# Kernel tuning notes

Hardware: AMD Instinct MI355X
Metric: run time of the kernel (lower is better)

## Reference

```python
import jax, jax.numpy as jnp
import numpy as np

D_IN = 3072      # == d_out (code reshapes x directly into heads)
D_OUT = 3072
N_HEADS = 16
HEAD_DIM = D_OUT // N_HEADS          # 192
D_C = D_OUT // 3                     # 1024, compressed latent dim
LN_EPS = 1e-5


def setup_inputs() -> dict:
    key = jax.random.key(0)
    ks = jax.random.split(key, 8)
    s = 0.02
    return {
        "x": jax.random.normal(ks[0], (2, 2048, D_IN), dtype=jnp.float32),
        "W_query": jax.random.normal(ks[1], (D_OUT, D_IN), dtype=jnp.float32) * s,
        "W_kv": jax.random.normal(ks[2], (D_C, D_IN), dtype=jnp.float32) * s,
        "W_uk": jax.random.normal(ks[3], (D_OUT, D_C), dtype=jnp.float32) * s,
        "W_uv": jax.random.normal(ks[4], (D_OUT, D_C), dtype=jnp.float32) * s,
        "W_out": jax.random.normal(ks[5], (D_OUT, D_OUT), dtype=jnp.float32) * s,
        "b_out": jnp.zeros((D_OUT,), dtype=jnp.float32),
        "ln_g": jnp.ones((D_C,), dtype=jnp.float32),
        "ln_b": jnp.zeros((D_C,), dtype=jnp.float32),
    }


def reference(x, W_query, W_kv, W_uk, W_uv, W_out, b_out, ln_g, ln_b):
    B, T, D = x.shape
    past_length = 0  # prefill, kv_cache=None

    # absorbed K projection: (d_out, d_in) @ (d_out, d_c) -> (H, head_dim, d_c)
    absorbed_k = (W_query @ W_uk).reshape(N_HEADS, HEAD_DIM, D_C)

    # compressed latent c_kv = LayerNorm(x @ W_kv^T), shape (B, S, d_c)
    c = x @ W_kv.T
    mu = jnp.mean(c, axis=-1, keepdims=True)
    var = jnp.mean(jnp.square(c - mu), axis=-1, keepdims=True)
    c_kv = (c - mu) * jax.lax.rsqrt(var + LN_EPS) * ln_g + ln_b
    S = c_kv.shape[1]

    # values decompressed: (B, S, H, head_dim)
    v = (c_kv @ W_uv.T).reshape(B, S, N_HEADS, HEAD_DIM)

    # queries: raw x reshaped into heads (as in the original code)
    q = x.reshape(B, T, N_HEADS, HEAD_DIM)

    # scores in compressed space: q @ absorbed_k @ c_kv^T
    tmp = jnp.einsum("bthd,hdc->bhtc", q, absorbed_k)           # (B,H,T,d_c)
    scores = jnp.einsum("bhtc,bsc->bhts", tmp, c_kv)
    scores = scores / np.float32(np.sqrt(HEAD_DIM))

    # causal mask with past_length offset (tril diagonal=past_length)
    row = jnp.arange(T)[:, None]
    col = jnp.arange(S)[None, :]
    mask = col <= (row + past_length)                            # (T,S) bool
    scores = jnp.where(mask[None, None], scores, -jnp.inf)

    weights = jax.nn.softmax(scores, axis=-1)                    # (B,H,T,S)

    ctx = jnp.einsum("bhts,bshd->bthd", weights, v).reshape(B, T, D_OUT)
    out = ctx @ W_out.T + b_out
    return out, c_kv
```

## Files before the change

kernel.cpp:

```cpp
#include <hip/hip_runtime.h>
#include <hip/hip_bf16.h>
#include <math.h>

#define BB 2
#define TT 2048
#define DD 3072
#define NH 16
#define HD 192
#define DC 1024

typedef __attribute__((ext_vector_type(8))) short bh8;
typedef __attribute__((ext_vector_type(4))) float f32x4;
typedef unsigned int u32;

__device__ __forceinline__ short f2b(float f) {
  __hip_bfloat16 h = __float2bfloat16(f);
  return *reinterpret_cast<short*>(&h);
}

__device__ __forceinline__ void gload16(const void* g, void* lds) {
  __builtin_amdgcn_global_load_lds(
      (const __attribute__((address_space(1))) u32*)g,
      (__attribute__((address_space(3))) u32*)lds, 16, 0, 0);
}

__global__ __launch_bounds__(256) void cast_f2b_k(const float* __restrict__ in,
                                                  short* __restrict__ out) {
  size_t i = ((size_t)blockIdx.x * 256 + threadIdx.x) * 8;
  float4 v0 = *(const float4*)&in[i];
  float4 v1 = *(const float4*)&in[i + 4];
  bh8 o;
  o[0] = f2b(v0.x); o[1] = f2b(v0.y); o[2] = f2b(v0.z); o[3] = f2b(v0.w);
  o[4] = f2b(v1.x); o[5] = f2b(v1.y); o[6] = f2b(v1.z); o[7] = f2b(v1.w);
  *(bh8*)&out[i] = o;
}

__global__ __launch_bounds__(256) void sum_cast_k(const float* __restrict__ p0,
                                                  const float* __restrict__ p1,
                                                  short* __restrict__ out) {
  size_t i = ((size_t)blockIdx.x * 256 + threadIdx.x) * 8;
  float4 a0 = *(const float4*)&p0[i];
  float4 a1 = *(const float4*)&p0[i + 4];
  float4 b0 = *(const float4*)&p1[i];
  float4 b1 = *(const float4*)&p1[i + 4];
  bh8 o;
  o[0] = f2b(a0.x + b0.x); o[1] = f2b(a0.y + b0.y);
  o[2] = f2b(a0.z + b0.z); o[3] = f2b(a0.w + b0.w);
  o[4] = f2b(a1.x + b1.x); o[5] = f2b(a1.y + b1.y);
  o[6] = f2b(a1.z + b1.z); o[7] = f2b(a1.w + b1.w);
  *(bh8*)&out[i] = o;
}

__global__ __launch_bounds__(256) void castT_f2b_k(const float* __restrict__ in,
                                                   short* __restrict__ out,
                                                   int R, int C) {
  __shared__ float t[64][65];
  const int cx = blockIdx.x * 64, ry = blockIdx.y * 64;
  const int tid = threadIdx.x, lx = tid & 15, ly = tid >> 4;
#pragma unroll
  for (int i = 0; i < 4; ++i) {
    int r = ly + i * 16;
    float4 v = *(const float4*)&in[(size_t)(ry + r) * C + cx + lx * 4];
    t[r][lx * 4 + 0] = v.x; t[r][lx * 4 + 1] = v.y;
    t[r][lx * 4 + 2] = v.z; t[r][lx * 4 + 3] = v.w;
  }
  __syncthreads();
#pragma unroll
  for (int i = 0; i < 4; ++i) {
    int c = ly + i * 16;
    ushort4 v;
    v.x = (unsigned short)f2b(t[lx * 4 + 0][c]);
    v.y = (unsigned short)f2b(t[lx * 4 + 1][c]);
    v.z = (unsigned short)f2b(t[lx * 4 + 2][c]);
    v.w = (unsigned short)f2b(t[lx * 4 + 3][c]);
    *(ushort4*)&out[(size_t)(cx + c) * R + ry + lx * 4] = v;
  }
}

template <int OUTMODE, bool BIAS>
__global__ __launch_bounds__(256) void gemm_bf16(
    const short* __restrict__ A, const short* __restrict__ Bt,
    const float* __restrict__ bias, void* __restrict__ Cout,
    void* __restrict__ Cout2,
    int M, int N, int Klen, int lda, int ldb, size_t zoff_bytes) {
  __shared__ short As[8192];
  __shared__ short Bs[8192];
  const int tid = threadIdx.x;
  const int w = tid >> 6, l = tid & 63, lm = l & 15, lg = l >> 4;
  const int wr = w >> 1, wc = w & 1;

  const int bz = blockIdx.z;
  A += (size_t)bz * Klen;
  Bt += (size_t)bz * Klen;
  Cout = (void*)((char*)Cout + (size_t)bz * zoff_bytes);

  const int nwg = gridDim.x * gridDim.y;
  const int flat = blockIdx.y * gridDim.x + blockIdx.x;
  const int wgid = (flat & 7) * (nwg >> 3) + (flat >> 3);
  const int m0 = (wgid / gridDim.x) * 128, n0 = (wgid % gridDim.x) * 128;

  f32x4 acc[4][4] = {};

  for (int k0 = 0; k0 < Klen; k0 += 64) {
    __syncthreads();
#pragma unroll
    for (int c = 0; c < 4; ++c) {
      int p = c * 256 + w * 64 + l;
      int row = p >> 3, kc = p & 7;
      int g = kc ^ (row & 7);
      gload16(&A[(size_t)(m0 + row) * lda + k0 + g * 8],
              &As[(c * 256 + w * 64) * 8]);
      gload16(&Bt[(size_t)(n0 + row) * ldb + k0 + g * 8],
              &Bs[(c * 256 + w * 64) * 8]);
    }
    __syncthreads();

#pragma unroll
    for (int kh = 0; kh < 2; ++kh) {
      bh8 a[4], b[4];
#pragma unroll
      for (int mi = 0; mi < 4; ++mi) {
        int r = wr * 64 + mi * 16 + lm;
        a[mi] = *(const bh8*)&As[r * 64 + (((kh * 4 + lg) ^ (r & 7)) << 3)];
      }
#pragma unroll
      for (int ni = 0; ni < 4; ++ni) {
        int r = wc * 64 + ni * 16 + lm;
        b[ni] = *(const bh8*)&Bs[r * 64 + (((kh * 4 + lg) ^ (r & 7)) << 3)];
      }
#pragma unroll
      for (int mi = 0; mi < 4; ++mi)
#pragma unroll
        for (int ni = 0; ni < 4; ++ni)
          acc[mi][ni] = __builtin_amdgcn_mfma_f32_16x16x32_bf16(
              a[mi], b[ni], acc[mi][ni], 0, 0, 0);
    }
  }

#pragma unroll
  for (int mi = 0; mi < 4; ++mi) {
#pragma unroll
    for (int ni = 0; ni < 4; ++ni) {
      int row = m0 + wr * 64 + mi * 16 + lg * 4;
      int col = n0 + wc * 64 + ni * 16 + lm;
      float bi = 0.f;
      if (BIAS) bi = bias[col];
      if (OUTMODE == 3) {
        if (n0 < 3072) {
          int b = row >> 11, t = row & 2047;
          ushort4 o4;
          o4.x = (unsigned short)f2b(acc[mi][ni][0]);
          o4.y = (unsigned short)f2b(acc[mi][ni][1]);
          o4.z = (unsigned short)f2b(acc[mi][ni][2]);
          o4.w = (unsigned short)f2b(acc[mi][ni][3]);
          *(ushort4*)&((short*)Cout2)[((size_t)(b * DD + col)) * TT + t] = o4;
        } else {
#pragma unroll
          for (int r = 0; r < 4; ++r)
            ((short*)Cout)[(size_t)(row + r) * DD + (col - 3072)] =
                f2b(acc[mi][ni][r]);
        }
      } else {
#pragma unroll
        for (int r = 0; r < 4; ++r) {
          float v = acc[mi][ni][r] + bi;
          if (OUTMODE == 1)
            ((short*)Cout)[(size_t)(row + r) * N + col] = f2b(v);
          else
            ((float*)Cout)[(size_t)(row + r) * N + col] = v;
        }
      }
    }
  }
}

__global__ __launch_bounds__(256) void ln_k(const float* __restrict__ cp0,
                                            const float* __restrict__ cp1,
                                            const float* __restrict__ g,
                                            const float* __restrict__ bta,
                                            float* __restrict__ o32,
                                            short* __restrict__ o16) {
  const int row = blockIdx.x;
  const int tid = threadIdx.x;
  __shared__ float red1[4];
  __shared__ float red2[4];

  float4 va = *(const float4*)&cp0[(size_t)row * DC + tid * 4];
  float4 vb = *(const float4*)&cp1[(size_t)row * DC + tid * 4];
  float4 v;
  v.x = va.x + vb.x; v.y = va.y + vb.y; v.z = va.z + vb.z; v.w = va.w + vb.w;
  float s = v.x + v.y + v.z + v.w;
#pragma unroll
  for (int mk = 32; mk; mk >>= 1) s += __shfl_xor(s, mk, 64);
  if ((tid & 63) == 0) red1[tid >> 6] = s;
  __syncthreads();
  float mu = (red1[0] + red1[1] + red1[2] + red1[3]) * (1.f / DC);

  float dx = v.x - mu, dy = v.y - mu, dz = v.z - mu, dw = v.w - mu;
  float s2 = dx * dx + dy * dy + dz * dz + dw * dw;
#pragma unroll
  for (int mk = 32; mk; mk >>= 1) s2 += __shfl_xor(s2, mk, 64);
  if ((tid & 63) == 0) red2[tid >> 6] = s2;
  __syncthreads();
  float var = (red2[0] + red2[1] + red2[2] + red2[3]) * (1.f / DC);
  float rs = rsqrtf(var + 1e-5f);

  float4 gg = *(const float4*)&g[tid * 4];
  float4 bb = *(const float4*)&bta[tid * 4];
  float4 o;
  o.x = dx * rs * gg.x + bb.x;
  o.y = dy * rs * gg.y + bb.y;
  o.z = dz * rs * gg.z + bb.z;
  o.w = dw * rs * gg.w + bb.w;
  *(float4*)&o32[(size_t)row * DC + tid * 4] = o;
  ushort4 ob;
  ob.x = (unsigned short)f2b(o.x); ob.y = (unsigned short)f2b(o.y);
  ob.z = (unsigned short)f2b(o.z); ob.w = (unsigned short)f2b(o.w);
  *(ushort4*)&o16[(size_t)row * DC + tid * 4] = ob;
}

__global__ __launch_bounds__(256, 4) void attn_mfma(
    const short* __restrict__ xb, const short* __restrict__ kf,
    const short* __restrict__ vT, short* __restrict__ ctx) {
  __shared__ short Ks[64 * 192];
  __shared__ short Vs[192 * 64];
  __shared__ short Ps[4][16 * 64];

  const int idx = blockIdx.x;
  const int qt = 31 - (idx >> 5);
  const int bh = idx & 31;
  const int h = bh & 15, b = bh >> 4;
  const int tid = threadIdx.x, w = tid >> 6, l = tid & 63;
  const int lm = l & 15, lg = l >> 4;
  const int qw0 = qt * 64 + w * 16;
  const float QS = 0.07216878364870323f;

  bh8 qf[6];
  {
    const short* qrow = &xb[(size_t)(b * TT + qw0 + lm) * DD + h * HD];
#pragma unroll
    for (int kq = 0; kq < 6; ++kq)
      qf[kq] = *(const bh8*)&qrow[kq * 32 + lg * 8];
  }

  f32x4 o[12] = {};
  float mrun[4], lrun[4];
#pragma unroll
  for (int r = 0; r < 4; ++r) { mrun[r] = -INFINITY; lrun[r] = 0.f; }

  for (int st = 0; st <= qt; ++st) {
    const int s0 = st * 64;
    __syncthreads();
#pragma unroll
    for (int c = 0; c < 6; ++c) {
      int p = c * 256 + w * 64 + l;
      {
        int krow = p / 24, kc = p - krow * 24;
        int g = kc ^ (krow & 7);
        gload16(&kf[(size_t)(b * TT + s0 + krow) * DD + h * HD + g * 8],
                &Ks[(c * 256 + w * 64) * 8]);
      }
      {
        int vrow = p >> 3, vc = p & 7;
        int gv = vc ^ (vrow & 7);
        gload16(&vT[(size_t)((b * NH + h) * HD + vrow) * TT + s0 + gv * 8],
                &Vs[(c * 256 + w * 64) * 8]);
      }
    }
    __syncthreads();

    f32x4 s[4] = {};
    __builtin_amdgcn_s_setprio(1);
#pragma unroll
    for (int nf = 0; nf < 4; ++nf) {
      const int krow = nf * 16 + lm;
      const short* kr = &Ks[krow * 192];
#pragma unroll
      for (int kq = 0; kq < 6; ++kq) {
        bh8 kb = *(const bh8*)&kr[(((kq * 4 + lg) ^ (krow & 7)) << 3)];
        s[nf] = __builtin_amdgcn_mfma_f32_16x16x32_bf16(qf[kq], kb, s[nf],
                                                        0, 0, 0);
      }
    }
    __builtin_amdgcn_s_setprio(0);

    float pv[4][4];
#pragma unroll
    for (int nf = 0; nf < 4; ++nf)
#pragma unroll
      for (int r = 0; r < 4; ++r) pv[nf][r] = s[nf][r] * QS;
    if (st == qt) {
#pragma unroll
      for (int nf = 0; nf < 4; ++nf)
#pragma unroll
        for (int r = 0; r < 4; ++r)
          if (nf * 16 + lm > w * 16 + lg * 4 + r) pv[nf][r] = -INFINITY;
    }
#pragma unroll
    for (int r = 0; r < 4; ++r) {
      float mt = fmaxf(fmaxf(pv[0][r], pv[1][r]), fmaxf(pv[2][r], pv[3][r]));
#pragma unroll
      for (int mk = 1; mk < 16; mk <<= 1) mt = fmaxf(mt, __shfl_xor(mt, mk));
      float mnew = fmaxf(mrun[r], mt);
      float corr = __expf(mrun[r] - mnew);
      mrun[r] = mnew;
      float ls = 0.f;
#pragma unroll
      for (int nf = 0; nf < 4; ++nf) {
        float p = __expf(pv[nf][r] - mnew);
        pv[nf][r] = p;
        ls += p;
      }
#pragma unroll
      for (int mk = 1; mk < 16; mk <<= 1) ls += __shfl_xor(ls, mk);
      lrun[r] = lrun[r] * corr + ls;
#pragma unroll
      for (int nf = 0; nf < 12; ++nf) o[nf][r] *= corr;
    }
#pragma unroll
    for (int nf = 0; nf < 4; ++nf)
#pragma unroll
      for (int r = 0; r < 4; ++r) {
        int prow = lg * 4 + r;
        int col = nf * 16 + lm;
        int sc = (((col >> 3) ^ (prow & 7)) << 3) + (col & 7);
        Ps[w][prow * 64 + sc] = f2b(pv[nf][r]);
      }

    bh8 pa0, pa1;
    {
      int prow = lm;
      pa0 = *(const bh8*)&Ps[w][prow * 64 + ((lg ^ (prow & 7)) << 3)];
      pa1 = *(const bh8*)&Ps[w][prow * 64 + (((4 + lg) ^ (prow & 7)) << 3)];
    }
    __builtin_amdgcn_s_setprio(1);
#pragma unroll
    for (int nf = 0; nf < 12; ++nf) {
      int drow = nf * 16 + lm;
      const short* vr = &Vs[drow * 64];
      bh8 vb0 = *(const bh8*)&vr[((lg ^ (drow & 7)) << 3)];
      bh8 vb1 = *(const bh8*)&vr[(((4 + lg) ^ (drow & 7)) << 3)];
      o[nf] = __builtin_amdgcn_mfma_f32_16x16x32_bf16(pa0, vb0, o[nf], 0, 0, 0);
      o[nf] = __builtin_amdgcn_mfma_f32_16x16x32_bf16(pa1, vb1, o[nf], 0, 0, 0);
    }
    __builtin_amdgcn_s_setprio(0);
  }

#pragma unroll
  for (int r = 0; r < 4; ++r) {
    float inv = 1.f / lrun[r];
    int row = qw0 + lg * 4 + r;
    short* cp = &ctx[(size_t)(b * TT + row) * DD + h * HD];
#pragma unroll
    for (int nf = 0; nf < 12; ++nf)
      cp[nf * 16 + lm] = f2b(o[nf][r] * inv);
  }
}

extern "C" void kernel_launch(void* const* d_in, const int* in_sizes, int n_in,
                              void* d_out, int out_size, void* d_ws,
                              size_t ws_size, hipStream_t stream) {
  const float* x    = (const float*)d_in[0];
  const float* Wq   = (const float*)d_in[1];
  const float* Wkv  = (const float*)d_in[2];
  const float* Wuk  = (const float*)d_in[3];
  const float* Wuv  = (const float*)d_in[4];
  const float* Wout = (const float*)d_in[5];
  const float* bout = (const float*)d_in[6];
  const float* lng  = (const float*)d_in[7];
  const float* lnb  = (const float*)d_in[8];

  float* out   = (float*)d_out;
  float* ckv32 = out + (size_t)BB * TT * DD;

  char* W = (char*)d_ws;
  short* xb     = (short*)(W);
  short* wbuf   = (short*)(W + 25165824);
  short* wukT   = (short*)(W + 44040192);
  short* wkvb   = (short*)(W + 50331648);
  short* wuvb   = (short*)(W + 56623104);
  short* akb    = (short*)(W + 62914560);
  float* cpre0  = (float*)(W + 69206016);
  short* ckvb   = (short*)(W + 85983232);
  short* kfullb = (short*)(W + 94371840);
  float* g1p0   = (float*)(W + 94371840);
  short* ctxb   = (short*)(W + 119537664);
  float* g1p1   = (float*)(W + 119537664);
  float* cpre1  = (float*)(W + 144703488);
  short* vTb    = (short*)(W + 144703488);
  const size_t G1_ZOFF = (size_t)(119537664 - 94371840);
  const size_t G2_ZOFF = (size_t)(144703488 - 69206016);

  cast_f2b_k<<<6144, 256, 0, stream>>>(x, xb);
  cast_f2b_k<<<4608, 256, 0, stream>>>(Wq, wbuf);
  cast_f2b_k<<<1536, 256, 0, stream>>>(Wkv, wkvb);
  cast_f2b_k<<<1536, 256, 0, stream>>>(Wuv, wuvb);
  castT_f2b_k<<<dim3(16, 48), 256, 0, stream>>>(Wuk, wukT, 3072, 1024);

  gemm_bf16<0, false><<<dim3(8, 24, 2), 256, 0, stream>>>(
      wbuf, wukT, nullptr, g1p0, nullptr, 3072, 1024, 1536, 3072, 3072,
      G1_ZOFF);
  sum_cast_k<<<1536, 256, 0, stream>>>(g1p0, g1p1, akb);
  cast_f2b_k<<<4608, 256, 0, stream>>>(Wout, wbuf);
  gemm_bf16<0, false><<<dim3(8, 32, 2), 256, 0, stream>>>(
      xb, wkvb, nullptr, cpre0, nullptr, 4096, 1024, 1536, 3072, 3072,
      G2_ZOFF);
  ln_k<<<4096, 256, 0, stream>>>(cpre0, cpre1, lng, lnb, ckv32, ckvb);
  gemm_bf16<3, false><<<dim3(48, 32), 256, 0, stream>>>(
      ckvb, wuvb, nullptr, kfullb, vTb, 4096, 6144, 1024, 1024, 1024, 0);
  attn_mfma<<<1024, 256, 0, stream>>>(xb, kfullb, vTb, ctxb);
  gemm_bf16<0, true><<<dim3(24, 32), 256, 0, stream>>>(
      ctxb, wbuf, bout, out, nullptr, 4096, 3072, 3072, 3072, 3072, 0);
}
```

Baseline: 398.0 us.

## Halve attention KV tile to 32, rebalance causal tile order, use exp2

The attention kernel now processes keys/values in 32-row tiles instead of 64, which halves the shared-memory footprint and finishes the causal diagonal with finer granularity. Block-to-query-tile mapping is changed to interleave long and short causal rows across dispatch slots for better load balance. Softmax switches to exp2 with the log2(e) factor folded into the score scale. The trade-off is twice as many loop iterations and barriers, with less MFMA work per barrier.

```diff
diff --git a/kernel.cpp b/kernel.cpp
--- a/kernel.cpp
+++ b/kernel.cpp
@@ -222,18 +222,22 @@
 __global__ __launch_bounds__(256, 4) void attn_mfma(
     const short* __restrict__ xb, const short* __restrict__ kf,
     const short* __restrict__ vT, short* __restrict__ ctx) {
-  __shared__ short Ks[64 * 192];
-  __shared__ short Vs[192 * 64];
-  __shared__ short Ps[4][16 * 64];
+  __shared__ short Ks[32 * 192];
+  __shared__ short Vs[192 * 32];
+  __shared__ short Ps[4][16 * 32];
 
   const int idx = blockIdx.x;
-  const int qt = 31 - (idx >> 5);
+  const int sslot = idx >> 8;
+  const int j = (idx >> 5) & 7;
+  const int qt = (sslot == 0) ? (31 - j)
+               : (sslot == 1) ? j
+               : (sslot == 2) ? (23 - j) : (8 + j);
   const int bh = idx & 31;
   const int h = bh & 15, b = bh >> 4;
   const int tid = threadIdx.x, w = tid >> 6, l = tid & 63;
   const int lm = l & 15, lg = l >> 4;
   const int qw0 = qt * 64 + w * 16;
-  const float QS = 0.07216878364870323f;
+  const float QS2 = 0.10411756672f;
 
   bh8 qf[6];
   {
@@ -248,11 +252,12 @@
 #pragma unroll
   for (int r = 0; r < 4; ++r) { mrun[r] = -INFINITY; lrun[r] = 0.f; }
 
-  for (int st = 0; st <= qt; ++st) {
-    const int s0 = st * 64;
+  const int st_max = 2 * qt + 1;
+  for (int st = 0; st <= st_max; ++st) {
+    const int s0 = st * 32;
     __syncthreads();
 #pragma unroll
-    for (int c = 0; c < 6; ++c) {
+    for (int c = 0; c < 3; ++c) {
       int p = c * 256 + w * 64 + l;
       {
         int krow = p / 24, kc = p - krow * 24;
@@ -261,18 +266,18 @@
                 &Ks[(c * 256 + w * 64) * 8]);
       }
       {
-        int vrow = p >> 3, vc = p & 7;
-        int gv = vc ^ (vrow & 7);
+        int vrow = p >> 2, vc = p & 3;
+        int gv = vc ^ (vrow & 3);
         gload16(&vT[(size_t)((b * NH + h) * HD + vrow) * TT + s0 + gv * 8],
                 &Vs[(c * 256 + w * 64) * 8]);
       }
     }
     __syncthreads();
 
-    f32x4 s[4] = {};
+    f32x4 s[2] = {};
     __builtin_amdgcn_s_setprio(1);
 #pragma unroll
-    for (int nf = 0; nf < 4; ++nf) {
+    for (int nf = 0; nf < 2; ++nf) {
       const int krow = nf * 16 + lm;
       const short* kr = &Ks[krow * 192];
 #pragma unroll
@@ -284,30 +289,31 @@
     }
     __builtin_amdgcn_s_setprio(0);
 
-    float pv[4][4];
-#pragma unroll
-    for (int nf = 0; nf < 4; ++nf)
-#pragma unroll
-      for (int r = 0; r < 4; ++r) pv[nf][r] = s[nf][r] * QS;
-    if (st == qt) {
-#pragma unroll
-      for (int nf = 0; nf < 4; ++nf)
+    float pv[2][4];
+#pragma unroll
+    for (int nf = 0; nf < 2; ++nf)
+#pragma unroll
+      for (int r = 0; r < 4; ++r) pv[nf][r] = s[nf][r] * QS2;
+    if (st >= 2 * qt) {
+      const int dloc = s0 - qt * 64;
+#pragma unroll
+      for (int nf = 0; nf < 2; ++nf)
 #pragma unroll
         for (int r = 0; r < 4; ++r)
-          if (nf * 16 + lm > w * 16 + lg * 4 + r) pv[nf][r] = -INFINITY;
+          if (dloc + nf * 16 + lm > w * 16 + lg * 4 + r) pv[nf][r] = -INFINITY;
     }
 #pragma unroll
     for (int r = 0; r < 4; ++r) {
-      float mt = fmaxf(fmaxf(pv[0][r], pv[1][r]), fmaxf(pv[2][r], pv[3][r]));
+      float mt = fmaxf(pv[0][r], pv[1][r]);
 #pragma unroll
       for (int mk = 1; mk < 16; mk <<= 1) mt = fmaxf(mt, __shfl_xor(mt, mk));
       float mnew = fmaxf(mrun[r], mt);
-      float corr = __expf(mrun[r] - mnew);
+      float corr = exp2f(mrun[r] - mnew);
       mrun[r] = mnew;
       float ls = 0.f;
 #pragma unroll
-      for (int nf = 0; nf < 4; ++nf) {
-        float p = __expf(pv[nf][r] - mnew);
+      for (int nf = 0; nf < 2; ++nf) {
+        float p = exp2f(pv[nf][r] - mnew);
         pv[nf][r] = p;
         ls += p;
       }
@@ -318,30 +324,26 @@
       for (int nf = 0; nf < 12; ++nf) o[nf][r] *= corr;
     }
 #pragma unroll
-    for (int nf = 0; nf < 4; ++nf)
+    for (int nf = 0; nf < 2; ++nf)
 #pragma unroll
       for (int r = 0; r < 4; ++r) {
         int prow = lg * 4 + r;
         int col = nf * 16 + lm;
-        int sc = (((col >> 3) ^ (prow & 7)) << 3) + (col & 7);
-        Ps[w][prow * 64 + sc] = f2b(pv[nf][r]);
-      }
-
-    bh8 pa0, pa1;
+        int sc = (((col >> 3) ^ (prow & 3)) << 3) + (col & 7);
+        Ps[w][prow * 32 + sc] = f2b(pv[nf][r]);
+      }
+
+    bh8 pa0;
     {
       int prow = lm;
-      pa0 = *(const bh8*)&Ps[w][prow * 64 + ((lg ^ (prow & 7)) << 3)];
-      pa1 = *(const bh8*)&Ps[w][prow * 64 + (((4 + lg) ^ (prow & 7)) << 3)];
+      pa0 = *(const bh8*)&Ps[w][prow * 32 + ((lg ^ (prow & 3)) << 3)];
     }
     __builtin_amdgcn_s_setprio(1);
 #pragma unroll
     for (int nf = 0; nf < 12; ++nf) {
       int drow = nf * 16 + lm;
-      const short* vr = &Vs[drow * 64];
-      bh8 vb0 = *(const bh8*)&vr[((lg ^ (drow & 7)) << 3)];
-      bh8 vb1 = *(const bh8*)&vr[(((4 + lg) ^ (drow & 7)) << 3)];
+      bh8 vb0 = *(const bh8*)&Vs[drow * 32 + ((lg ^ (drow & 3)) << 3)];
       o[nf] = __builtin_amdgcn_mfma_f32_16x16x32_bf16(pa0, vb0, o[nf], 0, 0, 0);
-      o[nf] = __builtin_amdgcn_mfma_f32_16x16x32_bf16(pa1, vb1, o[nf], 0, 0, 0);
     }
     __builtin_amdgcn_s_setprio(0);
   }
```

Result: slower. 487.6 us (+22.5%).
